# Kernel tuning notes

Measured on AMD Instinct MI355X. Metric: run time of the kernel, lower is better.

The kernel has to match this reference:

```python
import jax, jax.numpy as jnp
import numpy as np

WS = (7, 7)        # window size
SHIFT = (3, 3)     # shift size
NUM_HEADS = 12


def _relative_position_index(ws):
    ch, cw = np.arange(ws[0]), np.arange(ws[1])
    coords = np.stack(np.meshgrid(ch, cw, indexing='ij'))          # [2, wh, ww]
    cf = coords.reshape(2, -1)                                     # [2, wh*ww]
    rel = cf[:, :, None] - cf[:, None, :]                          # [2, T, T]
    rel = rel.transpose(1, 2, 0)
    rel[:, :, 0] += ws[0] - 1
    rel[:, :, 1] += ws[1] - 1
    rel[:, :, 0] *= 2 * ws[1] - 1
    return rel.sum(-1)                                             # [T, T]


def _attn_mask(pad_H, pad_W, ws, shift):
    # static construction of the shifted-window mask (numpy, per torch code)
    img = np.zeros((pad_H, pad_W), dtype=np.float32)
    h_slices = ((0, pad_H - ws[0]), (pad_H - ws[0], pad_H - shift[0]), (pad_H - shift[0], pad_H))
    w_slices = ((0, pad_W - ws[1]), (pad_W - ws[1], pad_W - shift[1]), (pad_W - shift[1], pad_W))
    cnt = 0
    for h0, h1 in h_slices:
        for w0, w1 in w_slices:
            img[h0:h1, w0:w1] = cnt
            cnt += 1
    nW = (pad_H // ws[0]) * (pad_W // ws[1])
    m = img.reshape(pad_H // ws[0], ws[0], pad_W // ws[1], ws[1])
    m = m.transpose(0, 2, 1, 3).reshape(nW, ws[0] * ws[1])
    diff = m[:, None, :] - m[:, :, None]
    return np.where(diff != 0, -100.0, 0.0).astype(np.float32)     # [nW, T, T]


def setup_inputs() -> dict:
    key = jax.random.key(0)
    ks = jax.random.split(key, 6)
    dim = 384
    return {
        'x': jax.random.normal(ks[0], (32, 56, 56, dim), dtype=jnp.float32),
        'qkv_weight': jax.random.normal(ks[1], (3 * dim, dim), dtype=jnp.float32) * 0.02,
        'qkv_bias': jax.random.normal(ks[2], (3 * dim,), dtype=jnp.float32) * 0.02,
        'proj_weight': jax.random.normal(ks[3], (dim, dim), dtype=jnp.float32) * 0.02,
        'proj_bias': jax.random.normal(ks[4], (dim,), dtype=jnp.float32) * 0.02,
        'rel_pos_bias_table': jax.random.normal(ks[5], ((2 * WS[0] - 1) * (2 * WS[1] - 1), NUM_HEADS), dtype=jnp.float32) * 0.02,
    }


def reference(x, qkv_weight, qkv_bias, proj_weight, proj_bias, rel_pos_bias_table):
    B, H, W, C = x.shape
    wh, ww = WS
    T = wh * ww
    nh = NUM_HEADS
    dh = C // nh

    pad_b = (wh - H % wh) % wh
    pad_r = (ww - W % ww) % ww
    x = jnp.pad(x, ((0, 0), (0, pad_b), (0, pad_r), (0, 0)))
    pad_H, pad_W = H + pad_b, W + pad_r
    shift = [SHIFT[0] if wh < pad_H else 0, SHIFT[1] if ww < pad_W else 0]

    # relative position bias [1, nh, T, T]
    rpi = _relative_position_index(WS)                               # static int index
    bias = rel_pos_bias_table[jnp.asarray(rpi.reshape(-1))].reshape(T, T, nh)
    bias = jnp.transpose(bias, (2, 0, 1))[None]

    if sum(shift) > 0:
        x = jnp.roll(x, (-shift[0], -shift[1]), axis=(1, 2))

    nH, nW_ = pad_H // wh, pad_W // ww
    num_windows = nH * nW_
    # window partition -> [B*num_windows, T, C]
    xw = x.reshape(B, nH, wh, nW_, ww, C).transpose(0, 1, 3, 2, 4, 5).reshape(B * num_windows, T, C)

    qkv = xw @ qkv_weight.T + qkv_bias                               # [Bn, T, 3C]
    qkv = qkv.reshape(B * num_windows, T, 3, nh, dh).transpose(2, 0, 3, 1, 4)
    q, k, v = qkv[0], qkv[1], qkv[2]                                 # [Bn, nh, T, dh]

    attn = jnp.einsum('bhtd,bhsd->bhts', q * (dh ** -0.5), k) + bias

    if sum(shift) > 0:
        mask = jnp.asarray(_attn_mask(pad_H, pad_W, WS, shift))      # [nW, T, T]
        attn = attn.reshape(B, num_windows, nh, T, T) + mask[None, :, None]
        attn = attn.reshape(B * num_windows, nh, T, T)

    attn = jax.nn.softmax(attn, axis=-1)
    out = jnp.einsum('bhts,bhsd->bhtd', attn, v)                     # [Bn, nh, T, dh]
    out = out.transpose(0, 2, 1, 3).reshape(B * num_windows, T, C)
    out = out @ proj_weight.T + proj_bias

    out = out.reshape(B, nH, nW_, wh, ww, C).transpose(0, 1, 3, 2, 4, 5).reshape(B, pad_H, pad_W, C)
    if sum(shift) > 0:
        out = jnp.roll(out, (shift[0], shift[1]), axis=(1, 2))
    return out[:, :H, :W, :]
```

## Files before the change

### kernel.cpp

```cpp
#include <hip/hip_runtime.h>


typedef __bf16 bf16;
typedef __bf16 bf16x8 __attribute__((ext_vector_type(8)));
typedef __bf16 bf16x4 __attribute__((ext_vector_type(4)));
typedef float f32x4 __attribute__((ext_vector_type(4)));

#define NWIN   2048
#define WHN    24576
#define GTOK   100352
#define QKV_SCALE 0.17677669529663687f

#define QB_OFF 0u
#define KB_OFF 77070336u
#define VT_OFF 154140672u
#define XG_OFF 242221056u
#define BM_OFF 319291392u
#define WQ_OFF 325582848u
#define WP_OFF 326467584u

__device__ inline void gld16(const bf16* g, bf16* l) {
  __builtin_amdgcn_global_load_lds(
      (const __attribute__((address_space(1))) void*)g,
      (__attribute__((address_space(3))) void*)l, 16, 0, 0);
}

__global__ __launch_bounds__(256) void k_gather(const float* __restrict__ x,
                                                bf16* __restrict__ xg) {
  int idx = blockIdx.x * 256 + threadIdx.x;
  int g = idx / 48, cg = idx - g * 48;
  int w = g / 49, t = g - w * 49;
  int b = w >> 6, wi = w & 63;
  int wy = wi >> 3, wx = wi & 7;
  int ty = t / 7, tx = t - ty * 7;
  int sy = wy * 7 + ty + 3; if (sy >= 56) sy -= 56;
  int sx = wx * 7 + tx + 3; if (sx >= 56) sx -= 56;
  const float* src = x + (size_t)((b * 56 + sy) * 56 + sx) * 384 + cg * 8;
  float4 a0 = *(const float4*)src;
  float4 a1 = *(const float4*)(src + 4);
  bf16x8 o;
  o[0] = (bf16)a0.x; o[1] = (bf16)a0.y; o[2] = (bf16)a0.z; o[3] = (bf16)a0.w;
  o[4] = (bf16)a1.x; o[5] = (bf16)a1.y; o[6] = (bf16)a1.z; o[7] = (bf16)a1.w;
  *(bf16x8*)(xg + (size_t)g * 384 + cg * 8) = o;
}

__global__ __launch_bounds__(256) void k_cvt(const float* __restrict__ wqkv,
                                             const float* __restrict__ wproj,
                                             bf16* __restrict__ wq,
                                             bf16* __restrict__ wp) {
  int idx = blockIdx.x * 256 + threadIdx.x;
  const float* src; bf16* dst; int off;
  if (idx < 55296) { src = wqkv; dst = wq; off = idx * 8; }
  else             { src = wproj; dst = wp; off = (idx - 55296) * 8; }
  float4 a0 = *(const float4*)(src + off);
  float4 a1 = *(const float4*)(src + off + 4);
  bf16x8 o;
  o[0] = (bf16)a0.x; o[1] = (bf16)a0.y; o[2] = (bf16)a0.z; o[3] = (bf16)a0.w;
  o[4] = (bf16)a1.x; o[5] = (bf16)a1.y; o[6] = (bf16)a1.z; o[7] = (bf16)a1.w;
  *(bf16x8*)(dst + off) = o;
}

__global__ __launch_bounds__(256) void k_bias(const float* __restrict__ table,
                                              bf16* __restrict__ bm) {
  int idx = blockIdx.x * 256 + threadIdx.x;
  int r = idx & 3;
  int lane = (idx >> 2) & 63;
  int c = (idx >> 8) & 3;
  int ts = (idx >> 10) & 3;
  int comb = idx >> 12;
  int h = comb % 12, wi = comb / 12;
  int i = ts * 16 + ((lane >> 4) << 2) + r;
  int j = c * 16 + (lane & 15);
  float v;
  if (j >= 49) v = -30000.f;
  else if (i >= 49) v = 0.f;
  else {
    int wy = wi >> 3, wx = wi & 7;
    int iy = i / 7, ix = i - iy * 7;
    int jy = j / 7, jx = j - jy * 7;
    int rel = (iy - jy + 6) * 13 + (ix - jx + 6);
    int gyi = wy * 7 + iy, gxi = wx * 7 + ix;
    int gyj = wy * 7 + jy, gxj = wx * 7 + jx;
    int ri = ((gyi < 49) ? 0 : ((gyi < 53) ? 1 : 2)) * 3 +
             ((gxi < 49) ? 0 : ((gxi < 53) ? 1 : 2));
    int rj = ((gyj < 49) ? 0 : ((gyj < 53) ? 1 : 2)) * 3 +
             ((gxj < 49) ? 0 : ((gxj < 53) ? 1 : 2));
    v = table[rel * 12 + h] + ((ri == rj) ? 0.f : -100.f);
  }
  bm[idx] = (bf16)v;
}

__global__ __launch_bounds__(256) void k_zpad(bf16* __restrict__ vtb) {
  int r = blockIdx.x * 256 + threadIdx.x;
  bf16* p = vtb + (size_t)r * 56 + 49;
#pragma unroll
  for (int i = 0; i < 7; ++i) p[i] = (bf16)0.0f;
}

__global__ __launch_bounds__(256, 3) void k_qkv(
    const bf16* __restrict__ xg, const bf16* __restrict__ wg,
    const float* __restrict__ bqkv, bf16* __restrict__ qb,
    bf16* __restrict__ kb, bf16* __restrict__ vtb) {
  __shared__ __align__(16) bf16 As[128 * 64];
  __shared__ __align__(16) bf16 Bs[128 * 64];

  int tid = threadIdx.x;
  int wv = tid >> 6, lane = tid & 63, l16 = lane & 15, q4 = lane >> 4;
  int wr = wv >> 1, wc = wv & 1;
  int nb = blockIdx.x;
  int m0 = blockIdx.y * 128;
  int n0 = nb * 128;

  int srow = lane >> 3;
  int scg = lane & 7;

  f32x4 acc[4][4];
#pragma unroll
  for (int a = 0; a < 4; ++a)
#pragma unroll
    for (int b = 0; b < 4; ++b) acc[a][b] = (f32x4){0.f, 0.f, 0.f, 0.f};

  for (int k0 = 0; k0 < 384; k0 += 64) {
    __syncthreads();
#pragma unroll
    for (int s = 0; s < 4; ++s) {
      int row = (wv * 4 + s) * 8 + srow;
      int gc = (scg ^ (row & 7)) * 8;
      gld16(xg + (size_t)(m0 + row) * 384 + k0 + gc, As + (wv * 4 + s) * 512);
      gld16(wg + (size_t)(n0 + row) * 384 + k0 + gc, Bs + (wv * 4 + s) * 512);
    }
    __syncthreads();
#pragma unroll
    for (int kk = 0; kk < 2; ++kk) {
      bf16x8 af[4], bfr[4];
#pragma unroll
      for (int mi = 0; mi < 4; ++mi) {
        int m = wr * 64 + mi * 16 + l16;
        int g = kk * 4 + q4;
        af[mi] = *(const bf16x8*)(As + m * 64 + ((g ^ (m & 7)) * 8));
      }
#pragma unroll
      for (int ci = 0; ci < 4; ++ci) {
        int n = wc * 64 + ci * 16 + l16;
        int g = kk * 4 + q4;
        bfr[ci] = *(const bf16x8*)(Bs + n * 64 + ((g ^ (n & 7)) * 8));
      }
#pragma unroll
      for (int mi = 0; mi < 4; ++mi)
#pragma unroll
        for (int ci = 0; ci < 4; ++ci)
          acc[mi][ci] =
              __builtin_amdgcn_mfma_f32_16x16x32_bf16(af[mi], bfr[ci], acc[mi][ci], 0, 0, 0);
    }
  }

  int which = nb / 3;
  float bias4[4]; int h4[4], d4[4];
#pragma unroll
  for (int ci = 0; ci < 4; ++ci) {
    int n = n0 + wc * 64 + ci * 16 + l16;
    bias4[ci] = bqkv[n];
    int hd = n - which * 384;
    h4[ci] = hd >> 5; d4[ci] = hd & 31;
  }
#pragma unroll
  for (int mi = 0; mi < 4; ++mi) {
#pragma unroll
    for (int r = 0; r < 4; ++r) {
      int mrow = m0 + wr * 64 + mi * 16 + q4 * 4 + r;
      int w = mrow / 49, tt = mrow - w * 49;
      int wb = w * 12;
#pragma unroll
      for (int ci = 0; ci < 4; ++ci) {
        float val = acc[mi][ci][r] + bias4[ci];
        int whi = wb + h4[ci];
        if (which == 0)
          qb[(size_t)(whi * 49 + tt) * 32 + d4[ci]] = (bf16)(val * QKV_SCALE);
        else if (which == 1)
          kb[(size_t)(whi * 49 + tt) * 32 + d4[ci]] = (bf16)val;
        else
          vtb[(size_t)(whi * 32 + d4[ci]) * 56 + tt] = (bf16)val;
      }
    }
  }
}

__global__ __launch_bounds__(256) void k_attn(
    const bf16* __restrict__ qb, const bf16* __restrict__ kb,
    const bf16* __restrict__ vtb, const bf16* __restrict__ bm,
    bf16* __restrict__ ab) {
  __shared__ __align__(16) bf16 P[4][16][72];

  int tid = threadIdx.x;
  int wv = tid >> 6, lane = tid & 63, l16 = lane & 15, q4 = lane >> 4;
  int whi = blockIdx.x * 4 + wv;
  int w = whi / 12, h = whi - w * 12;
  int wi = w & 63;

  const bf16* qq = qb + (size_t)whi * 1568;
  const bf16* kk = kb + (size_t)whi * 1568;
  const bf16* vv = vtb + (size_t)whi * 1792;
  const bf16* bmb = bm + ((size_t)(wi * 12 + h) << 12);

  bf16x8 z8;
#pragma unroll
  for (int i = 0; i < 8; ++i) z8[i] = (bf16)0.0f;

  bf16x8 kf[4];
#pragma unroll
  for (int c = 0; c < 4; ++c)
    kf[c] = *(const bf16x8*)(kk + (c * 16 + l16) * 32 + q4 * 8);
  bf16x8 v0[2], v1[2];
#pragma unroll
  for (int c2 = 0; c2 < 2; ++c2) {
    v0[c2] = *(const bf16x8*)(vv + (c2 * 16 + l16) * 56 + q4 * 8);
    v1[c2] = (q4 < 3) ? *(const bf16x8*)(vv + (c2 * 16 + l16) * 56 + 32 + q4 * 8)
                      : z8;
  }

  const f32x4 zero4 = {0.f, 0.f, 0.f, 0.f};

  for (int ts = 0; ts < 4; ++ts) {
    bf16x8 qf = *(const bf16x8*)(qq + (ts * 16 + l16) * 32 + q4 * 8);
    f32x4 s[4];
#pragma unroll
    for (int c = 0; c < 4; ++c)
      s[c] = __builtin_amdgcn_mfma_f32_16x16x32_bf16(qf, kf[c], zero4, 0, 0, 0);
#pragma unroll
    for (int c = 0; c < 4; ++c) {
      bf16x4 bv = *(const bf16x4*)(bmb + (ts * 4 + c) * 256 + lane * 4);
#pragma unroll
      for (int r = 0; r < 4; ++r) s[c][r] += (float)bv[r];
    }
#pragma unroll
    for (int r = 0; r < 4; ++r) {
      float m = fmaxf(fmaxf(s[0][r], s[1][r]), fmaxf(s[2][r], s[3][r]));
      m = fmaxf(m, __shfl_xor(m, 1));
      m = fmaxf(m, __shfl_xor(m, 2));
      m = fmaxf(m, __shfl_xor(m, 4));
      m = fmaxf(m, __shfl_xor(m, 8));
      float e0 = __expf(s[0][r] - m);
      float e1 = __expf(s[1][r] - m);
      float e2 = __expf(s[2][r] - m);
      float e3 = __expf(s[3][r] - m);
      float sm = e0 + e1 + e2 + e3;
      sm += __shfl_xor(sm, 1);
      sm += __shfl_xor(sm, 2);
      sm += __shfl_xor(sm, 4);
      sm += __shfl_xor(sm, 8);
      float inv = 1.0f / sm;
      int ir = q4 * 4 + r;
      P[wv][ir][l16] = (bf16)(e0 * inv);
      P[wv][ir][16 + l16] = (bf16)(e1 * inv);
      P[wv][ir][32 + l16] = (bf16)(e2 * inv);
      P[wv][ir][48 + l16] = (bf16)(e3 * inv);
    }
    __builtin_amdgcn_wave_barrier();
    bf16x8 p0 = *(const bf16x8*)&P[wv][l16][q4 * 8];
    bf16x8 p1 = *(const bf16x8*)&P[wv][l16][32 + q4 * 8];
    f32x4 o0 = __builtin_amdgcn_mfma_f32_16x16x32_bf16(p0, v0[0], zero4, 0, 0, 0);
    o0 = __builtin_amdgcn_mfma_f32_16x16x32_bf16(p1, v1[0], o0, 0, 0, 0);
    f32x4 o1 = __builtin_amdgcn_mfma_f32_16x16x32_bf16(p0, v0[1], zero4, 0, 0, 0);
    o1 = __builtin_amdgcn_mfma_f32_16x16x32_bf16(p1, v1[1], o1, 0, 0, 0);
    __builtin_amdgcn_wave_barrier();
#pragma unroll
    for (int r = 0; r < 4; ++r) {
      int i = ts * 16 + q4 * 4 + r;
      if (i < 49) {
        bf16* dst = ab + (size_t)(w * 49 + i) * 384 + h * 32;
        dst[l16] = (bf16)o0[r];
        dst[16 + l16] = (bf16)o1[r];
      }
    }
  }
}

__global__ __launch_bounds__(256, 3) void k_proj(
    const bf16* __restrict__ ab, const bf16* __restrict__ wp,
    const float* __restrict__ bp, float* __restrict__ out) {
  __shared__ __align__(16) bf16 As[128 * 64];
  __shared__ __align__(16) bf16 Bs[128 * 64];

  int tid = threadIdx.x;
  int wv = tid >> 6, lane = tid & 63, l16 = lane & 15, q4 = lane >> 4;
  int wr = wv >> 1, wc = wv & 1;
  int m0 = blockIdx.y * 128;
  int n0 = blockIdx.x * 128;

  int srow = lane >> 3;
  int scg = lane & 7;

  f32x4 acc[4][4];
#pragma unroll
  for (int a = 0; a < 4; ++a)
#pragma unroll
    for (int b = 0; b < 4; ++b) acc[a][b] = (f32x4){0.f, 0.f, 0.f, 0.f};

  for (int k0 = 0; k0 < 384; k0 += 64) {
    __syncthreads();
#pragma unroll
    for (int s = 0; s < 4; ++s) {
      int row = (wv * 4 + s) * 8 + srow;
      int gc = (scg ^ (row & 7)) * 8;
      gld16(ab + (size_t)(m0 + row) * 384 + k0 + gc, As + (wv * 4 + s) * 512);
      gld16(wp + (size_t)(n0 + row) * 384 + k0 + gc, Bs + (wv * 4 + s) * 512);
    }
    __syncthreads();
#pragma unroll
    for (int kk = 0; kk < 2; ++kk) {
      bf16x8 af[4], bfr[4];
#pragma unroll
      for (int mi = 0; mi < 4; ++mi) {
        int m = wr * 64 + mi * 16 + l16;
        int g = kk * 4 + q4;
        af[mi] = *(const bf16x8*)(As + m * 64 + ((g ^ (m & 7)) * 8));
      }
#pragma unroll
      for (int ci = 0; ci < 4; ++ci) {
        int n = wc * 64 + ci * 16 + l16;
        int g = kk * 4 + q4;
        bfr[ci] = *(const bf16x8*)(Bs + n * 64 + ((g ^ (n & 7)) * 8));
      }
#pragma unroll
      for (int mi = 0; mi < 4; ++mi)
#pragma unroll
        for (int ci = 0; ci < 4; ++ci)
          acc[mi][ci] =
              __builtin_amdgcn_mfma_f32_16x16x32_bf16(af[mi], bfr[ci], acc[mi][ci], 0, 0, 0);
    }
  }

  float bias4[4]; int col4[4];
#pragma unroll
  for (int ci = 0; ci < 4; ++ci) {
    col4[ci] = n0 + wc * 64 + ci * 16 + l16;
    bias4[ci] = bp[col4[ci]];
  }
#pragma unroll
  for (int mi = 0; mi < 4; ++mi) {
#pragma unroll
    for (int r = 0; r < 4; ++r) {
      int mrow = m0 + wr * 64 + mi * 16 + q4 * 4 + r;
      int w = mrow / 49, t = mrow - w * 49;
      int b = w >> 6, wi = w & 63;
      int wy = wi >> 3, wx = wi & 7;
      int ty = t / 7, tx = t - ty * 7;
      int gy = wy * 7 + ty + 3; if (gy >= 56) gy -= 56;
      int gx = wx * 7 + tx + 3; if (gx >= 56) gx -= 56;
      float* orow = out + (size_t)((b * 56 + gy) * 56 + gx) * 384;
#pragma unroll
      for (int ci = 0; ci < 4; ++ci) orow[col4[ci]] = acc[mi][ci][r] + bias4[ci];
    }
  }
}

extern "C" void kernel_launch(void* const* d_in, const int* in_sizes, int n_in,
                              void* d_out, int out_size, void* d_ws,
                              size_t ws_size, hipStream_t stream) {
  const float* x     = (const float*)d_in[0];
  const float* wqkv  = (const float*)d_in[1];
  const float* bqkv  = (const float*)d_in[2];
  const float* wproj = (const float*)d_in[3];
  const float* bproj = (const float*)d_in[4];
  const float* table = (const float*)d_in[5];
  float* out = (float*)d_out;

  char* ws = (char*)d_ws;
  bf16* qb  = (bf16*)(ws + QB_OFF);
  bf16* kb  = (bf16*)(ws + KB_OFF);
  bf16* vtb = (bf16*)(ws + VT_OFF);
  bf16* xg  = (bf16*)(ws + XG_OFF);
  bf16* ab  = (bf16*)(ws + XG_OFF);
  bf16* bmb = (bf16*)(ws + BM_OFF);
  bf16* wqg = (bf16*)(ws + WQ_OFF);
  bf16* wpg = (bf16*)(ws + WP_OFF);

  k_gather<<<dim3(18816), dim3(256), 0, stream>>>(x, xg);
  k_cvt<<<dim3(288), dim3(256), 0, stream>>>(wqkv, wproj, wqg, wpg);
  k_bias<<<dim3(12288), dim3(256), 0, stream>>>(table, bmb);
  k_zpad<<<dim3(3072), dim3(256), 0, stream>>>(vtb);
  k_qkv<<<dim3(9, 784), dim3(256), 0, stream>>>(xg, wqg, bqkv, qb, kb, vtb);
  k_attn<<<dim3(6144), dim3(256), 0, stream>>>(qb, kb, vtb, bmb, ab);
  k_proj<<<dim3(3, 784), dim3(256), 0, stream>>>(ab, wpg, bproj, out);
}
```

Baseline: 639.4 us.

## Merge prep kernels, store V untransposed, remap GEMM blocks across XCDs

Merges the gather, weight-convert and bias-table kernels into one launch and drops the V zero-pad kernel. V is now stored row-major like Q and K, and the attention kernel gathers the transposed B fragments with scalar loads. In the QKV write this turns the strided transposed store into contiguous stores, at the cost of uncoalesced 2-byte reads in attention. Both GEMMs get a 1D grid remapped so that consecutive M tiles land on the same XCD, aiming at better L2 reuse.

```diff
diff --git a/kernel.cpp b/kernel.cpp
--- a/kernel.cpp
+++ b/kernel.cpp
@@ -13,11 +13,11 @@
 
 #define QB_OFF 0u
 #define KB_OFF 77070336u
-#define VT_OFF 154140672u
-#define XG_OFF 242221056u
-#define BM_OFF 319291392u
-#define WQ_OFF 325582848u
-#define WP_OFF 326467584u
+#define VB_OFF 154140672u
+#define XG_OFF 231211008u
+#define BM_OFF 308281344u
+#define WQ_OFF 314572800u
+#define WP_OFF 315457536u
 
 __device__ inline void gld16(const bf16* g, bf16* l) {
   __builtin_amdgcn_global_load_lds(
@@ -25,90 +25,83 @@
       (__attribute__((address_space(3))) void*)l, 16, 0, 0);
 }
 
-__global__ __launch_bounds__(256) void k_gather(const float* __restrict__ x,
-                                                bf16* __restrict__ xg) {
-  int idx = blockIdx.x * 256 + threadIdx.x;
-  int g = idx / 48, cg = idx - g * 48;
-  int w = g / 49, t = g - w * 49;
-  int b = w >> 6, wi = w & 63;
-  int wy = wi >> 3, wx = wi & 7;
-  int ty = t / 7, tx = t - ty * 7;
-  int sy = wy * 7 + ty + 3; if (sy >= 56) sy -= 56;
-  int sx = wx * 7 + tx + 3; if (sx >= 56) sx -= 56;
-  const float* src = x + (size_t)((b * 56 + sy) * 56 + sx) * 384 + cg * 8;
-  float4 a0 = *(const float4*)src;
-  float4 a1 = *(const float4*)(src + 4);
-  bf16x8 o;
-  o[0] = (bf16)a0.x; o[1] = (bf16)a0.y; o[2] = (bf16)a0.z; o[3] = (bf16)a0.w;
-  o[4] = (bf16)a1.x; o[5] = (bf16)a1.y; o[6] = (bf16)a1.z; o[7] = (bf16)a1.w;
-  *(bf16x8*)(xg + (size_t)g * 384 + cg * 8) = o;
-}
-
-__global__ __launch_bounds__(256) void k_cvt(const float* __restrict__ wqkv,
-                                             const float* __restrict__ wproj,
-                                             bf16* __restrict__ wq,
-                                             bf16* __restrict__ wp) {
-  int idx = blockIdx.x * 256 + threadIdx.x;
-  const float* src; bf16* dst; int off;
-  if (idx < 55296) { src = wqkv; dst = wq; off = idx * 8; }
-  else             { src = wproj; dst = wp; off = (idx - 55296) * 8; }
-  float4 a0 = *(const float4*)(src + off);
-  float4 a1 = *(const float4*)(src + off + 4);
-  bf16x8 o;
-  o[0] = (bf16)a0.x; o[1] = (bf16)a0.y; o[2] = (bf16)a0.z; o[3] = (bf16)a0.w;
-  o[4] = (bf16)a1.x; o[5] = (bf16)a1.y; o[6] = (bf16)a1.z; o[7] = (bf16)a1.w;
-  *(bf16x8*)(dst + off) = o;
-}
-
-__global__ __launch_bounds__(256) void k_bias(const float* __restrict__ table,
-                                              bf16* __restrict__ bm) {
-  int idx = blockIdx.x * 256 + threadIdx.x;
-  int r = idx & 3;
-  int lane = (idx >> 2) & 63;
-  int c = (idx >> 8) & 3;
-  int ts = (idx >> 10) & 3;
-  int comb = idx >> 12;
-  int h = comb % 12, wi = comb / 12;
-  int i = ts * 16 + ((lane >> 4) << 2) + r;
-  int j = c * 16 + (lane & 15);
-  float v;
-  if (j >= 49) v = -30000.f;
-  else if (i >= 49) v = 0.f;
-  else {
+__global__ __launch_bounds__(256) void k_prep(
+    const float* __restrict__ x, const float* __restrict__ wqkv,
+    const float* __restrict__ wproj, const float* __restrict__ table,
+    bf16* __restrict__ xg, bf16* __restrict__ wq, bf16* __restrict__ wp,
+    bf16* __restrict__ bm) {
+  int blk = blockIdx.x;
+  if (blk < 18816) {
+    int idx = blk * 256 + threadIdx.x;
+    int g = idx / 48, cg = idx - g * 48;
+    int w = g / 49, t = g - w * 49;
+    int b = w >> 6, wi = w & 63;
     int wy = wi >> 3, wx = wi & 7;
-    int iy = i / 7, ix = i - iy * 7;
-    int jy = j / 7, jx = j - jy * 7;
-    int rel = (iy - jy + 6) * 13 + (ix - jx + 6);
-    int gyi = wy * 7 + iy, gxi = wx * 7 + ix;
-    int gyj = wy * 7 + jy, gxj = wx * 7 + jx;
-    int ri = ((gyi < 49) ? 0 : ((gyi < 53) ? 1 : 2)) * 3 +
-             ((gxi < 49) ? 0 : ((gxi < 53) ? 1 : 2));
-    int rj = ((gyj < 49) ? 0 : ((gyj < 53) ? 1 : 2)) * 3 +
-             ((gxj < 49) ? 0 : ((gxj < 53) ? 1 : 2));
-    v = table[rel * 12 + h] + ((ri == rj) ? 0.f : -100.f);
-  }
-  bm[idx] = (bf16)v;
-}
-
-__global__ __launch_bounds__(256) void k_zpad(bf16* __restrict__ vtb) {
-  int r = blockIdx.x * 256 + threadIdx.x;
-  bf16* p = vtb + (size_t)r * 56 + 49;
-#pragma unroll
-  for (int i = 0; i < 7; ++i) p[i] = (bf16)0.0f;
+    int ty = t / 7, tx = t - ty * 7;
+    int sy = wy * 7 + ty + 3; if (sy >= 56) sy -= 56;
+    int sx = wx * 7 + tx + 3; if (sx >= 56) sx -= 56;
+    const float* src = x + (size_t)((b * 56 + sy) * 56 + sx) * 384 + cg * 8;
+    float4 a0 = *(const float4*)src;
+    float4 a1 = *(const float4*)(src + 4);
+    bf16x8 o;
+    o[0] = (bf16)a0.x; o[1] = (bf16)a0.y; o[2] = (bf16)a0.z; o[3] = (bf16)a0.w;
+    o[4] = (bf16)a1.x; o[5] = (bf16)a1.y; o[6] = (bf16)a1.z; o[7] = (bf16)a1.w;
+    *(bf16x8*)(xg + (size_t)g * 384 + cg * 8) = o;
+  } else if (blk < 19104) {
+    int idx = (blk - 18816) * 256 + threadIdx.x;
+    const float* src; bf16* dst; int off;
+    if (idx < 55296) { src = wqkv; dst = wq; off = idx * 8; }
+    else             { src = wproj; dst = wp; off = (idx - 55296) * 8; }
+    float4 a0 = *(const float4*)(src + off);
+    float4 a1 = *(const float4*)(src + off + 4);
+    bf16x8 o;
+    o[0] = (bf16)a0.x; o[1] = (bf16)a0.y; o[2] = (bf16)a0.z; o[3] = (bf16)a0.w;
+    o[4] = (bf16)a1.x; o[5] = (bf16)a1.y; o[6] = (bf16)a1.z; o[7] = (bf16)a1.w;
+    *(bf16x8*)(dst + off) = o;
+  } else {
+    int idx = (blk - 19104) * 256 + threadIdx.x;
+    int r = idx & 3;
+    int lane = (idx >> 2) & 63;
+    int c = (idx >> 8) & 3;
+    int ts = (idx >> 10) & 3;
+    int comb = idx >> 12;
+    int h = comb % 12, wi = comb / 12;
+    int i = ts * 16 + ((lane >> 4) << 2) + r;
+    int j = c * 16 + (lane & 15);
+    float v;
+    if (j >= 49) v = -30000.f;
+    else if (i >= 49) v = 0.f;
+    else {
+      int wy = wi >> 3, wx = wi & 7;
+      int iy = i / 7, ix = i - iy * 7;
+      int jy = j / 7, jx = j - jy * 7;
+      int rel = (iy - jy + 6) * 13 + (ix - jx + 6);
+      int gyi = wy * 7 + iy, gxi = wx * 7 + ix;
+      int gyj = wy * 7 + jy, gxj = wx * 7 + jx;
+      int ri = ((gyi < 49) ? 0 : ((gyi < 53) ? 1 : 2)) * 3 +
+               ((gxi < 49) ? 0 : ((gxi < 53) ? 1 : 2));
+      int rj = ((gyj < 49) ? 0 : ((gyj < 53) ? 1 : 2)) * 3 +
+               ((gxj < 49) ? 0 : ((gxj < 53) ? 1 : 2));
+      v = table[rel * 12 + h] + ((ri == rj) ? 0.f : -100.f);
+    }
+    bm[idx] = (bf16)v;
+  }
 }
 
 __global__ __launch_bounds__(256, 3) void k_qkv(
     const bf16* __restrict__ xg, const bf16* __restrict__ wg,
     const float* __restrict__ bqkv, bf16* __restrict__ qb,
-    bf16* __restrict__ kb, bf16* __restrict__ vtb) {
+    bf16* __restrict__ kb, bf16* __restrict__ vb) {
   __shared__ __align__(16) bf16 As[128 * 64];
   __shared__ __align__(16) bf16 Bs[128 * 64];
 
   int tid = threadIdx.x;
   int wv = tid >> 6, lane = tid & 63, l16 = lane & 15, q4 = lane >> 4;
   int wr = wv >> 1, wc = wv & 1;
-  int nb = blockIdx.x;
-  int m0 = blockIdx.y * 128;
+  int bid = blockIdx.x;
+  int xcd = bid & 7, s = bid >> 3;
+  int nb = s % 9, mt = s / 9;
+  int m0 = (mt * 8 + xcd) * 128;
   int n0 = nb * 128;
 
   int srow = lane >> 3;
@@ -123,11 +116,11 @@
   for (int k0 = 0; k0 < 384; k0 += 64) {
     __syncthreads();
 #pragma unroll
-    for (int s = 0; s < 4; ++s) {
-      int row = (wv * 4 + s) * 8 + srow;
+    for (int st = 0; st < 4; ++st) {
+      int row = (wv * 4 + st) * 8 + srow;
       int gc = (scg ^ (row & 7)) * 8;
-      gld16(xg + (size_t)(m0 + row) * 384 + k0 + gc, As + (wv * 4 + s) * 512);
-      gld16(wg + (size_t)(n0 + row) * 384 + k0 + gc, Bs + (wv * 4 + s) * 512);
+      gld16(xg + (size_t)(m0 + row) * 384 + k0 + gc, As + (wv * 4 + st) * 512);
+      gld16(wg + (size_t)(n0 + row) * 384 + k0 + gc, Bs + (wv * 4 + st) * 512);
     }
     __syncthreads();
 #pragma unroll
@@ -173,13 +166,13 @@
 #pragma unroll
       for (int ci = 0; ci < 4; ++ci) {
         float val = acc[mi][ci][r] + bias4[ci];
-        int whi = wb + h4[ci];
+        size_t addr = (size_t)((wb + h4[ci]) * 49 + tt) * 32 + d4[ci];
         if (which == 0)
-          qb[(size_t)(whi * 49 + tt) * 32 + d4[ci]] = (bf16)(val * QKV_SCALE);
+          qb[addr] = (bf16)(val * QKV_SCALE);
         else if (which == 1)
-          kb[(size_t)(whi * 49 + tt) * 32 + d4[ci]] = (bf16)val;
+          kb[addr] = (bf16)val;
         else
-          vtb[(size_t)(whi * 32 + d4[ci]) * 56 + tt] = (bf16)val;
+          vb[addr] = (bf16)val;
       }
     }
   }
@@ -187,7 +180,7 @@
 
 __global__ __launch_bounds__(256) void k_attn(
     const bf16* __restrict__ qb, const bf16* __restrict__ kb,
-    const bf16* __restrict__ vtb, const bf16* __restrict__ bm,
+    const bf16* __restrict__ vb, const bf16* __restrict__ bm,
     bf16* __restrict__ ab) {
   __shared__ __align__(16) bf16 P[4][16][72];
 
@@ -199,24 +192,22 @@
 
   const bf16* qq = qb + (size_t)whi * 1568;
   const bf16* kk = kb + (size_t)whi * 1568;
-  const bf16* vv = vtb + (size_t)whi * 1792;
+  const bf16* vv = vb + (size_t)whi * 1568;
   const bf16* bmb = bm + ((size_t)(wi * 12 + h) << 12);
-
-  bf16x8 z8;
-#pragma unroll
-  for (int i = 0; i < 8; ++i) z8[i] = (bf16)0.0f;
 
   bf16x8 kf[4];
 #pragma unroll
   for (int c = 0; c < 4; ++c)
     kf[c] = *(const bf16x8*)(kk + (c * 16 + l16) * 32 + q4 * 8);
-  bf16x8 v0[2], v1[2];
-#pragma unroll
-  for (int c2 = 0; c2 < 2; ++c2) {
-    v0[c2] = *(const bf16x8*)(vv + (c2 * 16 + l16) * 56 + q4 * 8);
-    v1[c2] = (q4 < 3) ? *(const bf16x8*)(vv + (c2 * 16 + l16) * 56 + 32 + q4 * 8)
-                      : z8;
-  }
+
+  bf16x8 vf[2][2];
+#pragma unroll
+  for (int half = 0; half < 2; ++half)
+#pragma unroll
+    for (int c2 = 0; c2 < 2; ++c2)
+#pragma unroll
+      for (int j = 0; j < 8; ++j)
+        vf[half][c2][j] = vv[(half * 32 + q4 * 8 + j) * 32 + c2 * 16 + l16];
 
   const f32x4 zero4 = {0.f, 0.f, 0.f, 0.f};
 
@@ -258,10 +249,10 @@
     __builtin_amdgcn_wave_barrier();
     bf16x8 p0 = *(const bf16x8*)&P[wv][l16][q4 * 8];
     bf16x8 p1 = *(const bf16x8*)&P[wv][l16][32 + q4 * 8];
-    f32x4 o0 = __builtin_amdgcn_mfma_f32_16x16x32_bf16(p0, v0[0], zero4, 0, 0, 0);
-    o0 = __builtin_amdgcn_mfma_f32_16x16x32_bf16(p1, v1[0], o0, 0, 0, 0);
-    f32x4 o1 = __builtin_amdgcn_mfma_f32_16x16x32_bf16(p0, v0[1], zero4, 0, 0, 0);
-    o1 = __builtin_amdgcn_mfma_f32_16x16x32_bf16(p1, v1[1], o1, 0, 0, 0);
+    f32x4 o0 = __builtin_amdgcn_mfma_f32_16x16x32_bf16(p0, vf[0][0], zero4, 0, 0, 0);
+    o0 = __builtin_amdgcn_mfma_f32_16x16x32_bf16(p1, vf[1][0], o0, 0, 0, 0);
+    f32x4 o1 = __builtin_amdgcn_mfma_f32_16x16x32_bf16(p0, vf[0][1], zero4, 0, 0, 0);
+    o1 = __builtin_amdgcn_mfma_f32_16x16x32_bf16(p1, vf[1][1], o1, 0, 0, 0);
     __builtin_amdgcn_wave_barrier();
 #pragma unroll
     for (int r = 0; r < 4; ++r) {
@@ -284,8 +275,11 @@
   int tid = threadIdx.x;
   int wv = tid >> 6, lane = tid & 63, l16 = lane & 15, q4 = lane >> 4;
   int wr = wv >> 1, wc = wv & 1;
-  int m0 = blockIdx.y * 128;
-  int n0 = blockIdx.x * 128;
+  int bid = blockIdx.x;
+  int xcd = bid & 7, s = bid >> 3;
+  int nb = s % 3, mt = s / 3;
+  int m0 = (mt * 8 + xcd) * 128;
+  int n0 = nb * 128;
 
   int srow = lane >> 3;
   int scg = lane & 7;
@@ -299,11 +293,11 @@
   for (int k0 = 0; k0 < 384; k0 += 64) {
     __syncthreads();
 #pragma unroll
-    for (int s = 0; s < 4; ++s) {
-      int row = (wv * 4 + s) * 8 + srow;
+    for (int st = 0; st < 4; ++st) {
+      int row = (wv * 4 + st) * 8 + srow;
       int gc = (scg ^ (row & 7)) * 8;
-      gld16(ab + (size_t)(m0 + row) * 384 + k0 + gc, As + (wv * 4 + s) * 512);
-      gld16(wp + (size_t)(n0 + row) * 384 + k0 + gc, Bs + (wv * 4 + s) * 512);
+      gld16(ab + (size_t)(m0 + row) * 384 + k0 + gc, As + (wv * 4 + st) * 512);
+      gld16(wp + (size_t)(n0 + row) * 384 + k0 + gc, Bs + (wv * 4 + st) * 512);
     }
     __syncthreads();
 #pragma unroll
@@ -368,18 +362,16 @@
   char* ws = (char*)d_ws;
   bf16* qb  = (bf16*)(ws + QB_OFF);
   bf16* kb  = (bf16*)(ws + KB_OFF);
-  bf16* vtb = (bf16*)(ws + VT_OFF);
+  bf16* vb  = (bf16*)(ws + VB_OFF);
   bf16* xg  = (bf16*)(ws + XG_OFF);
   bf16* ab  = (bf16*)(ws + XG_OFF);
   bf16* bmb = (bf16*)(ws + BM_OFF);
   bf16* wqg = (bf16*)(ws + WQ_OFF);
   bf16* wpg = (bf16*)(ws + WP_OFF);
 
-  k_gather<<<dim3(18816), dim3(256), 0, stream>>>(x, xg);
-  k_cvt<<<dim3(288), dim3(256), 0, stream>>>(wqkv, wproj, wqg, wpg);
-  k_bias<<<dim3(12288), dim3(256), 0, stream>>>(table, bmb);
-  k_zpad<<<dim3(3072), dim3(256), 0, stream>>>(vtb);
-  k_qkv<<<dim3(9, 784), dim3(256), 0, stream>>>(xg, wqg, bqkv, qb, kb, vtb);
-  k_attn<<<dim3(6144), dim3(256), 0, stream>>>(qb, kb, vtb, bmb, ab);
-  k_proj<<<dim3(3, 784), dim3(256), 0, stream>>>(ab, wpg, bproj, out);
-}
+  k_prep<<<dim3(31392), dim3(256), 0, stream>>>(x, wqkv, wproj, table,
+                                                xg, wqg, wpg, bmb);
+  k_qkv<<<dim3(7056), dim3(256), 0, stream>>>(xg, wqg, bqkv, qb, kb, vb);
+  k_attn<<<dim3(6144), dim3(256), 0, stream>>>(qb, kb, vb, bmb, ab);
+  k_proj<<<dim3(2352), dim3(256), 0, stream>>>(ab, wpg, bproj, out);
+}
```

After: 524.2 us. 1.22x faster.
